# Performance work log

Hardware: AMD Instinct MI355X
Metric: run time of the kernel (lower is better)

## Reference

```python
import jax, jax.numpy as jnp
import numpy as np

B, C, H, W_IMG, P, D = 64, 3, 224, 224, 16, 768
N_PATCH = (H // P) * (W_IMG // P)  # 196
SEQ = N_PATCH + 1                  # 197


def setup_inputs() -> dict:
    key = jax.random.key(0)
    k1, k2, k3, k4, k5 = jax.random.split(key, 5)
    in_feat = P * P * C  # 768
    return {
        "x": jax.random.normal(k1, (B, C, H, W_IMG), dtype=jnp.float32),
        "W": jax.random.normal(k2, (in_feat, D), dtype=jnp.float32) * (1.0 / np.sqrt(in_feat)),
        "b": jax.random.normal(k3, (D,), dtype=jnp.float32) * 0.02,
        "pos_table": jax.random.normal(k4, (SEQ, D), dtype=jnp.float32) * 0.02,
        "class_token": jax.random.normal(k5, (1, 1, D), dtype=jnp.float32),
    }


def _patchify(x):
    # Matches torch loop: patch (i,j) is x[:, :, i*P:(i+1)*P, j*P:(j+1)*P].reshape(B, C*P*P)
    # i.e. features ordered channel-major then row then col within patch.
    b = x.shape[0]
    hp, wp = H // P, W_IMG // P
    x = x.reshape(b, C, hp, P, wp, P)              # (B,C,hp,P,wp,P)
    x = x.transpose(0, 2, 4, 1, 3, 5)              # (B,hp,wp,C,P,P)
    return x.reshape(b, hp * wp, C * P * P)        # (B,N,C*P*P)


def reference(x, W, b, pos_table, class_token):
    patches = _patchify(x)                          # (B, N, C*P*P)
    tokens = jnp.einsum("bnf,fd->bnd", patches, W) + b  # (B, N, D)
    cls = jnp.broadcast_to(class_token, (x.shape[0], 1, D))
    seq = jnp.concatenate([cls, tokens], axis=1)    # (B, SEQ, D)
    # positions = arange(SEQ) broadcast over batch -> embedding lookup
    return seq + pos_table[None, :, :]              # dropout is identity in eval
```

## Files before the change

kernel.cpp:

```cpp
#include <hip/hip_runtime.h>
#include <hip/hip_bf16.h>

namespace {

constexpr int Bsz = 64, Cch = 3, Himg = 224, Wimg = 224, Ppat = 16;
constexpr int Dm = 768, NPW = 14, NPATCH = 196, SEQn = 197;
constexpr int Mtot = Bsz * NPATCH;
constexpr int Ktot = 768, Ntot = 768;
constexpr int BM = 64, BN = 128, BK = 64;
constexpr int MT = Mtot / BM;
constexpr int NT = Ntot / BN;
constexpr int KT = Ktot / BK;
constexpr int NBLK = MT * NT;
constexpr int TA = BM * BK;
constexpr int TB = BN * BK;
constexpr size_t AP_ELEMS = (size_t)MT * KT * TA;
constexpr size_t WT_ELEMS = (size_t)NT * KT * TB;
constexpr size_t WS_NEED = (AP_ELEMS + WT_ELEMS) * 2;
constexpr int WPREP_BLK = (Ktot / 8) * Ntot / 256;
constexpr int CLS_BLK = Bsz * Dm / 256;

typedef __attribute__((ext_vector_type(8))) short bf16x8;
typedef __attribute__((ext_vector_type(4))) float f32x4;

__device__ inline unsigned short f2bf(float f) {
  __bf16 h = (__bf16)f;
  union { __bf16 h; unsigned short u; } c;
  c.h = h;
  return c.u;
}

__global__ void prep_kernel(const float* __restrict__ x, const float* __restrict__ W,
                            const float* __restrict__ pos, const float* __restrict__ cls,
                            unsigned short* __restrict__ Ap, unsigned short* __restrict__ Wt,
                            float* __restrict__ out, int nPatchBlk) {
  __shared__ unsigned short tile[TA];
  const int bid = blockIdx.x;
  const int t = threadIdx.x;
  if (bid < nPatchBlk) {
    int mt = bid / KT, kt = bid - mt * KT;
    int ml = t >> 2, ks = t & 3;
    int m = mt * BM + ml;
    int b = m / NPATCH;
    int pidx = m - b * NPATCH;
    int ph = pidx / NPW, pw = pidx - ph * NPW;
    int kbase = kt * BK + ks * 16;
    int c = kbase >> 8, pi = (kbase >> 4) & 15;
    const float* src = x + (((size_t)(b * Cch + c) * Himg + ph * Ppat + pi) * Wimg + pw * Ppat);
#pragma unroll
    for (int j = 0; j < 4; ++j) {
      float4 v = *reinterpret_cast<const float4*>(src + 4 * j);
      int idx = (ml * BK + ks * 16 + 4 * j) ^ ((ml & 7) << 3);
      *reinterpret_cast<ushort4*>(&tile[idx]) =
          make_ushort4(f2bf(v.x), f2bf(v.y), f2bf(v.z), f2bf(v.w));
    }
    __syncthreads();
    const uint4* sp = reinterpret_cast<const uint4*>(tile);
    uint4* dp = reinterpret_cast<uint4*>(Ap + (size_t)bid * TA);
    dp[t] = sp[t];
    dp[t + 256] = sp[t + 256];
  } else if (bid < nPatchBlk + WPREP_BLK) {
    int cid = (bid - nPatchBlk) * 256 + t;
    int kc = cid / Ntot;
    int n = cid - kc * Ntot;
    int nb = n >> 7;
    int np = n & 127;
    int kt = kc >> 3;
    int k8 = (kc & 7) * 8;
    unsigned short tmp[8];
#pragma unroll
    for (int j = 0; j < 8; ++j) tmp[j] = f2bf(W[(kc * 8 + j) * Ntot + n]);
    int idx = np * BK + k8;
    int sidx = idx ^ ((np & 7) << 3);
    unsigned short* dst = Wt + (size_t)(nb * KT + kt) * TB + sidx;
    *reinterpret_cast<ushort4*>(dst + 0) = make_ushort4(tmp[0], tmp[1], tmp[2], tmp[3]);
    *reinterpret_cast<ushort4*>(dst + 4) = make_ushort4(tmp[4], tmp[5], tmp[6], tmp[7]);
  } else {
    int i = (bid - nPatchBlk - WPREP_BLK) * 256 + t;
    int b = i / Dm;
    int d = i - b * Dm;
    out[(size_t)b * (SEQn * Dm) + d] = cls[d] + pos[d];
  }
}

__global__ __launch_bounds__(256, 2)
void gemm_kernel(const unsigned short* __restrict__ Ap, const unsigned short* __restrict__ Wt,
                 const float* __restrict__ bias, const float* __restrict__ pos,
                 float* __restrict__ out) {
  __shared__ unsigned short A[3][TA];
  __shared__ unsigned short B[3][TB];

  const int orig = blockIdx.x;
  const int wg = (orig & 7) * (NBLK / 8) + (orig >> 3);
  const int bm = wg / NT;
  const int bn = wg - bm * NT;

  const int t = threadIdx.x;
  const int lane = t & 63;
  const int wid = t >> 6;
  const int wr = wid >> 1, wc = wid & 1;
  const int fr = lane & 15, fq = lane >> 4;

  const unsigned short* aSrc = Ap + (size_t)(bm * KT) * TA + t * 8;
  const unsigned short* bSrc = Wt + (size_t)(bn * KT) * TB + t * 8;

  auto STAGE = [&](int buf, int kt) {
#pragma unroll
    for (int i = 0; i < 2; ++i)
      __builtin_amdgcn_global_load_lds(
          (const __attribute__((address_space(1))) unsigned int*)(aSrc + kt * TA + i * 2048),
          (__attribute__((address_space(3))) unsigned int*)(&A[buf][t * 8 + i * 2048]),
          16, 0, 0);
#pragma unroll
    for (int i = 0; i < 4; ++i)
      __builtin_amdgcn_global_load_lds(
          (const __attribute__((address_space(1))) unsigned int*)(bSrc + kt * TB + i * 2048),
          (__attribute__((address_space(3))) unsigned int*)(&B[buf][t * 8 + i * 2048]),
          16, 0, 0);
  };

  f32x4 acc[2][4];
#pragma unroll
  for (int mi = 0; mi < 2; ++mi)
#pragma unroll
    for (int ni = 0; ni < 4; ++ni) acc[mi][ni] = {0.f, 0.f, 0.f, 0.f};

  auto MFMA = [&](int cur) {
#pragma unroll
    for (int ks = 0; ks < 2; ++ks) {
      bf16x8 af[2], bfr[4];
#pragma unroll
      for (int mi = 0; mi < 2; ++mi) {
        int row = wr * 32 + mi * 16 + fr;
        int idx = (row * BK + ks * 32 + fq * 8) ^ ((row & 7) << 3);
        af[mi] = *reinterpret_cast<const bf16x8*>(&A[cur][idx]);
      }
#pragma unroll
      for (int ni = 0; ni < 4; ++ni) {
        int n = wc * 64 + ni * 16 + fr;
        int idx = (n * BK + ks * 32 + fq * 8) ^ ((n & 7) << 3);
        bfr[ni] = *reinterpret_cast<const bf16x8*>(&B[cur][idx]);
      }
#pragma unroll
      for (int mi = 0; mi < 2; ++mi)
#pragma unroll
        for (int ni = 0; ni < 4; ++ni)
          acc[mi][ni] = __builtin_amdgcn_mfma_f32_16x16x32_bf16(
              af[mi], bfr[ni], acc[mi][ni], 0, 0, 0);
    }
  };

  STAGE(0, 0);
  STAGE(1, 1);
#pragma unroll
  for (int kt = 0; kt < KT; ++kt) {
    if (kt + 1 < KT) {
      asm volatile("s_waitcnt vmcnt(6)" ::: "memory");
    } else {
      asm volatile("s_waitcnt vmcnt(0)" ::: "memory");
    }
    __builtin_amdgcn_s_barrier();
    if (kt + 2 < KT) STAGE((kt + 2) % 3, kt + 2);
    MFMA(kt % 3);
  }

  const int n0 = bn * BN + wc * 64;
  float bv[4];
#pragma unroll
  for (int ni = 0; ni < 4; ++ni) bv[ni] = bias[n0 + ni * 16 + fr];
#pragma unroll
  for (int mi = 0; mi < 2; ++mi) {
#pragma unroll
    for (int j = 0; j < 4; ++j) {
      int m = bm * BM + wr * 32 + mi * 16 + fq * 4 + j;
      int b = m / NPATCH;
      int s = m - b * NPATCH + 1;
      float* orow = out + ((size_t)b * SEQn + s) * Dm + n0;
      const float* prow = pos + (size_t)s * Dm + n0;
#pragma unroll
      for (int ni = 0; ni < 4; ++ni) {
        int d = ni * 16 + fr;
        orow[d] = acc[mi][ni][j] + bv[ni] + prow[d];
      }
    }
  }
}

__global__ __launch_bounds__(512, 6)
void gemm_fb(const float* __restrict__ x, const unsigned short* __restrict__ Wt,
             const float* __restrict__ bias, const float* __restrict__ pos,
             float* __restrict__ out) {
  __shared__ unsigned short As[2][TA];
  __shared__ unsigned short Bs[2][TB];

  const int orig = blockIdx.x;
  const int wg = (orig & 7) * (NBLK / 8) + (orig >> 3);
  const int bm = wg / NT;
  const int bn = wg - bm * NT;

  const int t = threadIdx.x;
  const int lane = t & 63;
  const int wid = t >> 6;
  const int wr = wid >> 2, wc = wid & 3;
  const int fr = lane & 15, fq = lane >> 4;

  const int c4 = t & 15;
  const int r0 = t >> 4;
  int a_base[2];
#pragma unroll
  for (int i = 0; i < 2; ++i) {
    int m = bm * BM + r0 + 32 * i;
    int b = m / NPATCH;
    int pidx = m - b * NPATCH;
    int ph = pidx / NPW;
    int pw = pidx - ph * NPW;
    a_base[i] = ((b * Cch) * Himg + ph * Ppat) * Wimg + pw * Ppat;
  }
  const unsigned short* wt_base = Wt + (size_t)bn * (KT * TB);

  float4 av[2];
  auto LOADA = [&](int kt) {
    int kg = kt * BK + c4 * 4;
    int c = kg >> 8;
    int pi = (kg >> 4) & 15;
    int pj = kg & 15;
    int off = (c * Himg + pi) * Wimg + pj;
#pragma unroll
    for (int i = 0; i < 2; ++i)
      av[i] = *reinterpret_cast<const float4*>(x + a_base[i] + off);
  };
  auto WRITEA = [&](int buf) {
#pragma unroll
    for (int i = 0; i < 2; ++i) {
      int row = r0 + 32 * i;
      int idx = (row * BK + c4 * 4) ^ ((row & 7) << 3);
      ushort4 pk = make_ushort4(f2bf(av[i].x), f2bf(av[i].y), f2bf(av[i].z), f2bf(av[i].w));
      *reinterpret_cast<ushort4*>(&As[buf][idx]) = pk;
    }
  };
  auto STAGEB = [&](int buf, int kt) {
    const unsigned short* src = wt_base + kt * TB + t * 8;
#pragma unroll
    for (int i = 0; i < 2; ++i) {
      __builtin_amdgcn_global_load_lds(
          (const __attribute__((address_space(1))) unsigned int*)(src + i * 4096),
          (__attribute__((address_space(3))) unsigned int*)(&Bs[buf][t * 8 + i * 4096]),
          16, 0, 0);
    }
  };

  f32x4 acc[2][2];
#pragma unroll
  for (int mi = 0; mi < 2; ++mi)
#pragma unroll
    for (int ni = 0; ni < 2; ++ni) acc[mi][ni] = {0.f, 0.f, 0.f, 0.f};

  LOADA(0);
  STAGEB(0, 0);
  WRITEA(0);
  __syncthreads();

  for (int kt = 0; kt < KT; ++kt) {
    const int cur = kt & 1, nxt = cur ^ 1;
    if (kt + 1 < KT) {
      LOADA(kt + 1);
      STAGEB(nxt, kt + 1);
    }
#pragma unroll
    for (int ks = 0; ks < 2; ++ks) {
      bf16x8 af[2], bfr[2];
#pragma unroll
      for (int mi = 0; mi < 2; ++mi) {
        int row = wr * 32 + mi * 16 + fr;
        int idx = (row * BK + ks * 32 + fq * 8) ^ ((row & 7) << 3);
        af[mi] = *reinterpret_cast<const bf16x8*>(&As[cur][idx]);
      }
#pragma unroll
      for (int ni = 0; ni < 2; ++ni) {
        int n = wc * 32 + ni * 16 + fr;
        int idx = (n * BK + ks * 32 + fq * 8) ^ ((n & 7) << 3);
        bfr[ni] = *reinterpret_cast<const bf16x8*>(&Bs[cur][idx]);
      }
#pragma unroll
      for (int mi = 0; mi < 2; ++mi)
#pragma unroll
        for (int ni = 0; ni < 2; ++ni)
          acc[mi][ni] = __builtin_amdgcn_mfma_f32_16x16x32_bf16(
              af[mi], bfr[ni], acc[mi][ni], 0, 0, 0);
    }
    if (kt + 1 < KT) WRITEA(nxt);
    __syncthreads();
  }

  const int n0 = bn * BN + wc * 32;
  float bv[2];
#pragma unroll
  for (int ni = 0; ni < 2; ++ni) bv[ni] = bias[n0 + ni * 16 + fr];
#pragma unroll
  for (int mi = 0; mi < 2; ++mi) {
#pragma unroll
    for (int j = 0; j < 4; ++j) {
      int m = bm * BM + wr * 32 + mi * 16 + fq * 4 + j;
      int b = m / NPATCH;
      int s = m - b * NPATCH + 1;
      float* orow = out + ((size_t)b * SEQn + s) * Dm + n0;
      const float* prow = pos + (size_t)s * Dm + n0;
#pragma unroll
      for (int ni = 0; ni < 2; ++ni) {
        int d = ni * 16 + fr;
        orow[d] = acc[mi][ni][j] + bv[ni] + prow[d];
      }
    }
  }
}

}

extern "C" void kernel_launch(void* const* d_in, const int* in_sizes, int n_in,
                              void* d_out, int out_size, void* d_ws, size_t ws_size,
                              hipStream_t stream) {
  const float* x = (const float*)d_in[0];
  const float* W = (const float*)d_in[1];
  const float* bias = (const float*)d_in[2];
  const float* pos = (const float*)d_in[3];
  const float* cls = (const float*)d_in[4];
  float* out = (float*)d_out;

  const bool pure = ws_size >= WS_NEED;
  unsigned short* Ap = (unsigned short*)d_ws;
  unsigned short* Wt = pure ? Ap + AP_ELEMS : Ap;
  const int nPatchBlk = pure ? MT * KT : 0;

  prep_kernel<<<nPatchBlk + WPREP_BLK + CLS_BLK, 256, 0, stream>>>(
      x, W, pos, cls, Ap, Wt, out, nPatchBlk);
  if (pure)
    gemm_kernel<<<NBLK, 256, 0, stream>>>(Ap, Wt, bias, pos, out);
  else
    gemm_fb<<<NBLK, 512, 0, stream>>>(x, Wt, bias, pos, out);
}
```

Before: 46.40 us.

## Load MFMA fragments directly from global memory in fragment-friendly K-major layout

The prep kernel now writes the patch matrix and transposed weights in a K-tile-major, row-contiguous layout with 16-byte stores, dropping the LDS staging tile. The GEMM loads bf16x8 MFMA fragments straight from global/L2 into registers, with no LDS buffers, no global_load_lds pipeline and no barriers, and allows three blocks per SIMD group. The goal is to remove LDS traffic and synchronisation overhead. The trade-offs are redundant global loads across waves, which lean on L2/cache bandwidth, and loss of the explicit prefetch pipelining. The fallback kernel is also reshaped to 256 threads and reads B directly from global.

New measurement: 99.86 us. +115.2%, slower.

```diff
diff --git a/kernel.cpp b/kernel.cpp
--- a/kernel.cpp
+++ b/kernel.cpp
@@ -12,12 +12,11 @@
 constexpr int NT = Ntot / BN;
 constexpr int KT = Ktot / BK;
 constexpr int NBLK = MT * NT;
-constexpr int TA = BM * BK;
-constexpr int TB = BN * BK;
-constexpr size_t AP_ELEMS = (size_t)MT * KT * TA;
-constexpr size_t WT_ELEMS = (size_t)NT * KT * TB;
+constexpr size_t AP_ELEMS = (size_t)KT * Mtot * BK;
+constexpr size_t WT_ELEMS = (size_t)KT * Ntot * BK;
 constexpr size_t WS_NEED = (AP_ELEMS + WT_ELEMS) * 2;
-constexpr int WPREP_BLK = (Ktot / 8) * Ntot / 256;
+constexpr int PATCH_BLK = MT * KT;
+constexpr int WPREP_BLK = KT * Ntot * 8 / 256;
 constexpr int CLS_BLK = Bsz * Dm / 256;
 
 typedef __attribute__((ext_vector_type(8))) short bf16x8;
@@ -30,51 +29,45 @@
   return c.u;
 }
 
+union Pack8 { unsigned short s[8]; uint4 v; };
+
 __global__ void prep_kernel(const float* __restrict__ x, const float* __restrict__ W,
                             const float* __restrict__ pos, const float* __restrict__ cls,
                             unsigned short* __restrict__ Ap, unsigned short* __restrict__ Wt,
                             float* __restrict__ out, int nPatchBlk) {
-  __shared__ unsigned short tile[TA];
   const int bid = blockIdx.x;
   const int t = threadIdx.x;
   if (bid < nPatchBlk) {
     int mt = bid / KT, kt = bid - mt * KT;
-    int ml = t >> 2, ks = t & 3;
-    int m = mt * BM + ml;
-    int b = m / NPATCH;
-    int pidx = m - b * NPATCH;
-    int ph = pidx / NPW, pw = pidx - ph * NPW;
-    int kbase = kt * BK + ks * 16;
-    int c = kbase >> 8, pi = (kbase >> 4) & 15;
-    const float* src = x + (((size_t)(b * Cch + c) * Himg + ph * Ppat + pi) * Wimg + pw * Ppat);
-#pragma unroll
-    for (int j = 0; j < 4; ++j) {
-      float4 v = *reinterpret_cast<const float4*>(src + 4 * j);
-      int idx = (ml * BK + ks * 16 + 4 * j) ^ ((ml & 7) << 3);
-      *reinterpret_cast<ushort4*>(&tile[idx]) =
-          make_ushort4(f2bf(v.x), f2bf(v.y), f2bf(v.z), f2bf(v.w));
-    }
-    __syncthreads();
-    const uint4* sp = reinterpret_cast<const uint4*>(tile);
-    uint4* dp = reinterpret_cast<uint4*>(Ap + (size_t)bid * TA);
-    dp[t] = sp[t];
-    dp[t + 256] = sp[t + 256];
+#pragma unroll
+    for (int it = 0; it < 2; ++it) {
+      int r = (t >> 3) + 32 * it;
+      int c8 = t & 7;
+      int m = mt * BM + r;
+      int b = m / NPATCH;
+      int pidx = m - b * NPATCH;
+      int ph = pidx / NPW, pw = pidx - ph * NPW;
+      int k0 = kt * BK + c8 * 8;
+      int c = k0 >> 8, pi = (k0 >> 4) & 15, pj = k0 & 15;
+      const float* src = x + (((size_t)(b * Cch + c) * Himg + ph * Ppat + pi) * Wimg
+                              + pw * Ppat + pj);
+      float4 v0 = *reinterpret_cast<const float4*>(src);
+      float4 v1 = *reinterpret_cast<const float4*>(src + 4);
+      Pack8 p;
+      p.s[0] = f2bf(v0.x); p.s[1] = f2bf(v0.y); p.s[2] = f2bf(v0.z); p.s[3] = f2bf(v0.w);
+      p.s[4] = f2bf(v1.x); p.s[5] = f2bf(v1.y); p.s[6] = f2bf(v1.z); p.s[7] = f2bf(v1.w);
+      *reinterpret_cast<uint4*>(Ap + (size_t)kt * Mtot * BK + (size_t)m * BK + c8 * 8) = p.v;
+    }
   } else if (bid < nPatchBlk + WPREP_BLK) {
     int cid = (bid - nPatchBlk) * 256 + t;
-    int kc = cid / Ntot;
-    int n = cid - kc * Ntot;
-    int nb = n >> 7;
-    int np = n & 127;
-    int kt = kc >> 3;
-    int k8 = (kc & 7) * 8;
-    unsigned short tmp[8];
-#pragma unroll
-    for (int j = 0; j < 8; ++j) tmp[j] = f2bf(W[(kc * 8 + j) * Ntot + n]);
-    int idx = np * BK + k8;
-    int sidx = idx ^ ((np & 7) << 3);
-    unsigned short* dst = Wt + (size_t)(nb * KT + kt) * TB + sidx;
-    *reinterpret_cast<ushort4*>(dst + 0) = make_ushort4(tmp[0], tmp[1], tmp[2], tmp[3]);
-    *reinterpret_cast<ushort4*>(dst + 4) = make_ushort4(tmp[4], tmp[5], tmp[6], tmp[7]);
+    int kt = cid / (Ntot * 8);
+    int rem = cid - kt * (Ntot * 8);
+    int n = rem >> 3;
+    int k8 = (rem & 7) * 8;
+    Pack8 p;
+#pragma unroll
+    for (int j = 0; j < 8; ++j) p.s[j] = f2bf(W[(size_t)(kt * BK + k8 + j) * Ntot + n]);
+    *reinterpret_cast<uint4*>(Wt + (size_t)kt * Ntot * BK + (size_t)n * BK + k8) = p.v;
   } else {
     int i = (bid - nPatchBlk - WPREP_BLK) * 256 + t;
     int b = i / Dm;
@@ -83,13 +76,10 @@
   }
 }
 
-__global__ __launch_bounds__(256, 2)
+__global__ __launch_bounds__(256, 3)
 void gemm_kernel(const unsigned short* __restrict__ Ap, const unsigned short* __restrict__ Wt,
                  const float* __restrict__ bias, const float* __restrict__ pos,
                  float* __restrict__ out) {
-  __shared__ unsigned short A[3][TA];
-  __shared__ unsigned short B[3][TB];
-
   const int orig = blockIdx.x;
   const int wg = (orig & 7) * (NBLK / 8) + (orig >> 3);
   const int bm = wg / NT;
@@ -101,23 +91,8 @@
   const int wr = wid >> 1, wc = wid & 1;
   const int fr = lane & 15, fq = lane >> 4;
 
-  const unsigned short* aSrc = Ap + (size_t)(bm * KT) * TA + t * 8;
-  const unsigned short* bSrc = Wt + (size_t)(bn * KT) * TB + t * 8;
-
-  auto STAGE = [&](int buf, int kt) {
-#pragma unroll
-    for (int i = 0; i < 2; ++i)
-      __builtin_amdgcn_global_load_lds(
-          (const __attribute__((address_space(1))) unsigned int*)(aSrc + kt * TA + i * 2048),
-          (__attribute__((address_space(3))) unsigned int*)(&A[buf][t * 8 + i * 2048]),
-          16, 0, 0);
-#pragma unroll
-    for (int i = 0; i < 4; ++i)
-      __builtin_amdgcn_global_load_lds(
-          (const __attribute__((address_space(1))) unsigned int*)(bSrc + kt * TB + i * 2048),
-          (__attribute__((address_space(3))) unsigned int*)(&B[buf][t * 8 + i * 2048]),
-          16, 0, 0);
-  };
+  const size_t aOff = (size_t)(bm * BM + wr * 32 + fr) * BK + fq * 8;
+  const size_t bOff = (size_t)(bn * BN + wc * 64 + fr) * BK + fq * 8;
 
   f32x4 acc[2][4];
 #pragma unroll
@@ -125,43 +100,29 @@
 #pragma unroll
     for (int ni = 0; ni < 4; ++ni) acc[mi][ni] = {0.f, 0.f, 0.f, 0.f};
 
-  auto MFMA = [&](int cur) {
-#pragma unroll
-    for (int ks = 0; ks < 2; ++ks) {
-      bf16x8 af[2], bfr[4];
-#pragma unroll
-      for (int mi = 0; mi < 2; ++mi) {
-        int row = wr * 32 + mi * 16 + fr;
-        int idx = (row * BK + ks * 32 + fq * 8) ^ ((row & 7) << 3);
-        af[mi] = *reinterpret_cast<const bf16x8*>(&A[cur][idx]);
-      }
-#pragma unroll
-      for (int ni = 0; ni < 4; ++ni) {
-        int n = wc * 64 + ni * 16 + fr;
-        int idx = (n * BK + ks * 32 + fq * 8) ^ ((n & 7) << 3);
-        bfr[ni] = *reinterpret_cast<const bf16x8*>(&B[cur][idx]);
-      }
+#pragma unroll 3
+  for (int kt = 0; kt < KT; ++kt) {
+    const unsigned short* aT = Ap + (size_t)kt * Mtot * BK + aOff;
+    const unsigned short* bT = Wt + (size_t)kt * Ntot * BK + bOff;
+    bf16x8 af[2][2], bf[4][2];
+#pragma unroll
+    for (int mi = 0; mi < 2; ++mi)
+#pragma unroll
+      for (int ks = 0; ks < 2; ++ks)
+        af[mi][ks] = *reinterpret_cast<const bf16x8*>(aT + (size_t)mi * 16 * BK + ks * 32);
+#pragma unroll
+    for (int ni = 0; ni < 4; ++ni)
+#pragma unroll
+      for (int ks = 0; ks < 2; ++ks)
+        bf[ni][ks] = *reinterpret_cast<const bf16x8*>(bT + (size_t)ni * 16 * BK + ks * 32);
+#pragma unroll
+    for (int ks = 0; ks < 2; ++ks)
 #pragma unroll
       for (int mi = 0; mi < 2; ++mi)
 #pragma unroll
         for (int ni = 0; ni < 4; ++ni)
           acc[mi][ni] = __builtin_amdgcn_mfma_f32_16x16x32_bf16(
-              af[mi], bfr[ni], acc[mi][ni], 0, 0, 0);
-    }
-  };
-
-  STAGE(0, 0);
-  STAGE(1, 1);
-#pragma unroll
-  for (int kt = 0; kt < KT; ++kt) {
-    if (kt + 1 < KT) {
-      asm volatile("s_waitcnt vmcnt(6)" ::: "memory");
-    } else {
-      asm volatile("s_waitcnt vmcnt(0)" ::: "memory");
-    }
-    __builtin_amdgcn_s_barrier();
-    if (kt + 2 < KT) STAGE((kt + 2) % 3, kt + 2);
-    MFMA(kt % 3);
+              af[mi][ks], bf[ni][ks], acc[mi][ni], 0, 0, 0);
   }
 
   const int n0 = bn * BN + wc * 64;
@@ -186,12 +147,11 @@
   }
 }
 
-__global__ __launch_bounds__(512, 6)
+__global__ __launch_bounds__(256, 2)
 void gemm_fb(const float* __restrict__ x, const unsigned short* __restrict__ Wt,
              const float* __restrict__ bias, const float* __restrict__ pos,
              float* __restrict__ out) {
-  __shared__ unsigned short As[2][TA];
-  __shared__ unsigned short Bs[2][TB];
+  __shared__ unsigned short As[2][BM * BK];
 
   const int orig = blockIdx.x;
   const int wg = (orig & 7) * (NBLK / 8) + (orig >> 3);
@@ -201,101 +161,87 @@
   const int t = threadIdx.x;
   const int lane = t & 63;
   const int wid = t >> 6;
-  const int wr = wid >> 2, wc = wid & 3;
+  const int wr = wid >> 1, wc = wid & 1;
   const int fr = lane & 15, fq = lane >> 4;
 
   const int c4 = t & 15;
   const int r0 = t >> 4;
-  int a_base[2];
-#pragma unroll
-  for (int i = 0; i < 2; ++i) {
-    int m = bm * BM + r0 + 32 * i;
+  int a_base[4];
+#pragma unroll
+  for (int i = 0; i < 4; ++i) {
+    int m = bm * BM + r0 + 16 * i;
     int b = m / NPATCH;
     int pidx = m - b * NPATCH;
     int ph = pidx / NPW;
     int pw = pidx - ph * NPW;
     a_base[i] = ((b * Cch) * Himg + ph * Ppat) * Wimg + pw * Ppat;
   }
-  const unsigned short* wt_base = Wt + (size_t)bn * (KT * TB);
-
-  float4 av[2];
+
+  float4 av[4];
   auto LOADA = [&](int kt) {
     int kg = kt * BK + c4 * 4;
-    int c = kg >> 8;
-    int pi = (kg >> 4) & 15;
-    int pj = kg & 15;
+    int c = kg >> 8, pi = (kg >> 4) & 15, pj = kg & 15;
     int off = (c * Himg + pi) * Wimg + pj;
 #pragma unroll
-    for (int i = 0; i < 2; ++i)
+    for (int i = 0; i < 4; ++i)
       av[i] = *reinterpret_cast<const float4*>(x + a_base[i] + off);
   };
   auto WRITEA = [&](int buf) {
 #pragma unroll
-    for (int i = 0; i < 2; ++i) {
-      int row = r0 + 32 * i;
+    for (int i = 0; i < 4; ++i) {
+      int row = r0 + 16 * i;
       int idx = (row * BK + c4 * 4) ^ ((row & 7) << 3);
       ushort4 pk = make_ushort4(f2bf(av[i].x), f2bf(av[i].y), f2bf(av[i].z), f2bf(av[i].w));
       *reinterpret_cast<ushort4*>(&As[buf][idx]) = pk;
     }
   };
-  auto STAGEB = [&](int buf, int kt) {
-    const unsigned short* src = wt_base + kt * TB + t * 8;
-#pragma unroll
-    for (int i = 0; i < 2; ++i) {
-      __builtin_amdgcn_global_load_lds(
-          (const __attribute__((address_space(1))) unsigned int*)(src + i * 4096),
-          (__attribute__((address_space(3))) unsigned int*)(&Bs[buf][t * 8 + i * 4096]),
-          16, 0, 0);
-    }
-  };
-
-  f32x4 acc[2][2];
+
+  const size_t bOff = (size_t)(bn * BN + wc * 64 + fr) * BK + fq * 8;
+
+  f32x4 acc[2][4];
 #pragma unroll
   for (int mi = 0; mi < 2; ++mi)
 #pragma unroll
-    for (int ni = 0; ni < 2; ++ni) acc[mi][ni] = {0.f, 0.f, 0.f, 0.f};
+    for (int ni = 0; ni < 4; ++ni) acc[mi][ni] = {0.f, 0.f, 0.f, 0.f};
 
   LOADA(0);
-  STAGEB(0, 0);
   WRITEA(0);
   __syncthreads();
 
   for (int kt = 0; kt < KT; ++kt) {
     const int cur = kt & 1, nxt = cur ^ 1;
-    if (kt + 1 < KT) {
-      LOADA(kt + 1);
-      STAGEB(nxt, kt + 1);
-    }
-#pragma unroll
-    for (int ks = 0; ks < 2; ++ks) {
-      bf16x8 af[2], bfr[2];
-#pragma unroll
-      for (int mi = 0; mi < 2; ++mi) {
+    if (kt + 1 < KT) LOADA(kt + 1);
+    const unsigned short* bT = Wt + (size_t)kt * Ntot * BK + bOff;
+    bf16x8 af[2][2], bf[4][2];
+#pragma unroll
+    for (int mi = 0; mi < 2; ++mi)
+#pragma unroll
+      for (int ks = 0; ks < 2; ++ks) {
         int row = wr * 32 + mi * 16 + fr;
         int idx = (row * BK + ks * 32 + fq * 8) ^ ((row & 7) << 3);
-        af[mi] = *reinterpret_cast<const bf16x8*>(&As[cur][idx]);
+        af[mi][ks] = *reinterpret_cast<const bf16x8*>(&As[cur][idx]);
       }
 #pragma unroll
-      for (int ni = 0; ni < 2; ++ni) {
-        int n = wc * 32 + ni * 16 + fr;
-        int idx = (n * BK + ks * 32 + fq * 8) ^ ((n & 7) << 3);
-        bfr[ni] = *reinterpret_cast<const bf16x8*>(&Bs[cur][idx]);
-      }
+    for (int ni = 0; ni < 4; ++ni)
+#pragma unroll
+      for (int ks = 0; ks < 2; ++ks)
+        bf[ni][ks] = *reinterpret_cast<const bf16x8*>(bT + (size_t)ni * 16 * BK + ks * 32);
+#pragma unroll
+    for (int ks = 0; ks < 2; ++ks)
 #pragma unroll
       for (int mi = 0; mi < 2; ++mi)
 #pragma unroll
-        for (int ni = 0; ni < 2; ++ni)
+        for (int ni = 0; ni < 4; ++ni)
           acc[mi][ni] = __builtin_amdgcn_mfma_f32_16x16x32_bf16(
-              af[mi], bfr[ni], acc[mi][ni], 0, 0, 0);
-    }
+              af[mi][ks], bf[ni][ks], acc[mi][ni], 0, 0, 0);
     if (kt + 1 < KT) WRITEA(nxt);
     __syncthreads();
   }
 
-  const int n0 = bn * BN + wc * 32;
-  float bv[2];
-#pragma unroll
-  for (int ni = 0; ni < 2; ++ni) bv[ni] = bias[n0 + ni * 16 + fr];
+  const int n0 = bn * BN + wc * 64;
+  float bv[4];
+#pragma unroll
+  for (int ni = 0; ni < 4; ++ni) bv[ni] = bias[n0 + ni * 16 + fr];
 #pragma unroll
   for (int mi = 0; mi < 2; ++mi) {
 #pragma unroll
@@ -306,7 +252,7 @@
       float* orow = out + ((size_t)b * SEQn + s) * Dm + n0;
       const float* prow = pos + (size_t)s * Dm + n0;
 #pragma unroll
-      for (int ni = 0; ni < 2; ++ni) {
+      for (int ni = 0; ni < 4; ++ni) {
         int d = ni * 16 + fr;
         orow[d] = acc[mi][ni][j] + bv[ni] + prow[d];
       }
@@ -329,12 +275,12 @@
   const bool pure = ws_size >= WS_NEED;
   unsigned short* Ap = (unsigned short*)d_ws;
   unsigned short* Wt = pure ? Ap + AP_ELEMS : Ap;
-  const int nPatchBlk = pure ? MT * KT : 0;
+  const int nPatchBlk = pure ? PATCH_BLK : 0;
 
   prep_kernel<<<nPatchBlk + WPREP_BLK + CLS_BLK, 256, 0, stream>>>(
       x, W, pos, cls, Ap, Wt, out, nPatchBlk);
   if (pure)
     gemm_kernel<<<NBLK, 256, 0, stream>>>(Ap, Wt, bias, pos, out);
   else
-    gemm_fb<<<NBLK, 512, 0, stream>>>(x, Wt, bias, pos, out);
-}
+    gemm_fb<<<NBLK, 256, 0, stream>>>(x, Wt, bias, pos, out);
+}
```
